# Kernel tuning notes

Hardware: AMD Instinct MI355X
Metric: run time of the kernel (lower is better)

## Reference

```python
import jax, jax.numpy as jnp
import numpy as np

D_MODEL = 768
NUM_HEADS = 6
SPARSITY = 0.1
HEAD_DIM = D_MODEL // NUM_HEADS
SCALE = HEAD_DIM ** -0.5
B, C = 8, 4096


def setup_inputs() -> dict:
    key = jax.random.key(0)
    k1, k2 = jax.random.split(key, 2)
    x = jax.random.normal(k1, (B, C, D_MODEL), dtype=jnp.float32)
    # to_qkv: Linear(d_model, 3*d_model); torch layout W:[out,in], b:[out]
    W = jax.random.normal(k2, (3 * D_MODEL, D_MODEL), dtype=jnp.float32) * (D_MODEL ** -0.5)
    b = jnp.zeros((3 * D_MODEL,), dtype=jnp.float32)
    return {"x": x, "W": W, "b": b}


def reference(x, W, b):
    Bb, Cc, X = x.shape
    H, Dh = NUM_HEADS, HEAD_DIM
    n = Bb * Cc
    qkv = (x.reshape(n, X) @ W.T + b).reshape(n, 3, H, Dh)
    q, k, v = qkv[:, 0], qkv[:, 1], qkv[:, 2]  # each [n, H, Dh]
    # per-token attention across heads: [n, H, H]
    scores = jnp.einsum('nhd,ngd->nhg', q, k) * SCALE
    k_heads = max(1, int(H * SPARSITY))
    topk_scores, topk_idx = jax.lax.top_k(scores, k_heads)  # [n, H, k]
    soft = jax.nn.softmax(topk_scores, axis=-1)
    # sparse_attn @ v == weighted gather of v rows at topk_idx (zeros elsewhere)
    v_g = jnp.take_along_axis(v[:, None, :, :], topk_idx[..., None], axis=2)  # [n, H, k, Dh]
    out = jnp.einsum('nhk,nhkd->nhd', soft, v_g)  # [n, H, Dh]
    # torch: out.transpose(1, 2).reshape(B, C, d_model)  (3D tensor -> swap H and Dh)
    out = jnp.swapaxes(out, 1, 2).reshape(Bb, Cc, X)
    channel_importance = jnp.linalg.norm(out, axis=-1)  # [B, C]
    k_channels = max(1, int(Cc * SPARSITY))
    _, ch_idx = jax.lax.top_k(channel_importance, k_channels)  # [B, k_channels]
    sparse_feat = jnp.take_along_axis(out, ch_idx[:, :, None], axis=1)  # [B, k_channels, d_model]
    return sparse_feat, ch_idx, k_channels
```

## Files before the change

kernel.cpp:

```cpp
#include <hip/hip_runtime.h>
#include <cstdint>
#include <cstddef>

#pragma clang fp contract(off)

#define NROWS 32768
#define NCOLS 2304
#define DMODEL 768
#define QK 1536
#define KCH 409
#define NBATCH 8
#define FEAT_ELEMS ((size_t)NBATCH * KCH * DMODEL)
#define SCALE_F 0.08838834764831845f

#define BM 128
#define BN 128
#define BK 32
#define RS 140

typedef float v4f __attribute__((ext_vector_type(4)));

__device__ __forceinline__ int chunk_off(int c) { return 8 * c + 4 * (c >> 2); }

__global__ __launch_bounds__(256) void gemm_qkv_f32(
    const float* __restrict__ x, const float* __restrict__ W,
    const float* __restrict__ bias, float* __restrict__ qkv)
{
    __shared__ float As[BK * RS];
    __shared__ float Bs[BK * RS];

    const int tid = threadIdx.x;
    const int tx = tid & 15;
    const int ty = tid >> 4;
    const int n0 = blockIdx.x * BN;
    const int m0 = blockIdx.y * BM;

    const int sm = tid >> 3;
    const int t8 = tid & 7;
    const int wsub = sm & 7;
    const int wchk = sm >> 3;

    const float* xa = x + (size_t)(m0 + sm) * DMODEL + t8;
    const float* wb = W + (size_t)(n0 + sm) * DMODEL + t8;

    int co[4];
    #pragma unroll
    for (int i = 0; i < 4; ++i) co[i] = chunk_off(wchk + 4 * i) + wsub;

    float pa[4][4], pb[4][4];
    #pragma unroll
    for (int i = 0; i < 4; ++i)
        #pragma unroll
        for (int j = 0; j < 4; ++j) {
            pa[i][j] = xa[(size_t)(32 * i) * DMODEL + 8 * j];
            pb[i][j] = wb[(size_t)(32 * i) * DMODEL + 8 * j];
        }

    float acc[8][8] = {};

    for (int kt = 0; kt < DMODEL / BK; ++kt) {
        __syncthreads();
        #pragma unroll
        for (int i = 0; i < 4; ++i) {
            #pragma unroll
            for (int j = 0; j < 4; ++j) {
                As[(t8 + 8 * j) * RS + co[i]] = pa[i][j];
                Bs[(t8 + 8 * j) * RS + co[i]] = pb[i][j];
            }
        }
        __syncthreads();

        if (kt + 1 < DMODEL / BK) {
            const int ko = (kt + 1) * BK;
            #pragma unroll
            for (int i = 0; i < 4; ++i)
                #pragma unroll
                for (int j = 0; j < 4; ++j) {
                    pa[i][j] = xa[(size_t)(32 * i) * DMODEL + ko + 8 * j];
                    pb[i][j] = wb[(size_t)(32 * i) * DMODEL + ko + 8 * j];
                }
        }

        const float* Ap = &As[chunk_off(ty)];
        const float* Bp = &Bs[chunk_off(tx)];
        #pragma unroll 8
        for (int k = 0; k < BK; ++k) {
            const v4f a0 = *(const v4f*)(Ap + k * RS);
            const v4f a1 = *(const v4f*)(Ap + k * RS + 4);
            const v4f b0 = *(const v4f*)(Bp + k * RS);
            const v4f b1 = *(const v4f*)(Bp + k * RS + 4);
            const float a[8] = {a0.x, a0.y, a0.z, a0.w, a1.x, a1.y, a1.z, a1.w};
            const float b[8] = {b0.x, b0.y, b0.z, b0.w, b1.x, b1.y, b1.z, b1.w};
            #pragma unroll
            for (int i = 0; i < 8; ++i)
                #pragma unroll
                for (int j = 0; j < 8; ++j)
                    acc[i][j] = fmaf(a[i], b[j], acc[i][j]);
        }
    }

    const int col = n0 + 8 * tx;
    float bcol[8];
    #pragma unroll
    for (int j = 0; j < 8; ++j) bcol[j] = bias[col + j];

    #pragma unroll
    for (int i = 0; i < 8; ++i) {
        const int row = m0 + 8 * ty + i;
        float4 o0, o1;
        o0.x = acc[i][0] + bcol[0];
        o0.y = acc[i][1] + bcol[1];
        o0.z = acc[i][2] + bcol[2];
        o0.w = acc[i][3] + bcol[3];
        o1.x = acc[i][4] + bcol[4];
        o1.y = acc[i][5] + bcol[5];
        o1.z = acc[i][6] + bcol[6];
        o1.w = acc[i][7] + bcol[7];
        *(float4*)(&qkv[(size_t)row * NCOLS + col])     = o0;
        *(float4*)(&qkv[(size_t)row * NCOLS + col + 4]) = o1;
    }
}

__global__ __launch_bounds__(256) void select_and_norm(
    const float* __restrict__ qkv, float* __restrict__ norms,
    uint64_t* __restrict__ gstar)
{
    __shared__ float rowbuf[4][NCOLS];
    __shared__ float sc[4][36];
    __shared__ int   gs_s[4][6];
    __shared__ float sblk[4][8];

    const int tid  = threadIdx.x;
    const int wave = tid >> 6;
    const int lane = tid & 63;
    const int n = blockIdx.x * 4 + wave;

    {
        const float4* src = (const float4*)(qkv + (size_t)n * NCOLS);
        float4* dst = (float4*)(&rowbuf[wave][0]);
        #pragma unroll
        for (int i = 0; i < 9; ++i) dst[lane + 64 * i] = src[lane + 64 * i];
    }
    __syncthreads();

    if (lane < 36) {
        const int h = lane / 6, g = lane % 6;
        const float* qh = &rowbuf[wave][h * 128];
        const float* kh = &rowbuf[wave][768 + g * 128];
        float s = 0.0f;
        for (int d = 0; d < 128; ++d)
            s = s + qh[d] * kh[d];
        sc[wave][lane] = s * SCALE_F;
    }
    __syncthreads();

    if (lane < 6) {
        float best = sc[wave][lane * 6];
        int bg = 0;
        #pragma unroll
        for (int g = 1; g < 6; ++g) {
            const float v = sc[wave][lane * 6 + g];
            if (v > best) { best = v; bg = g; }
        }
        gs_s[wave][lane] = bg;
    }
    __syncthreads();

    if (lane < 8) {
        const float* vr = &rowbuf[wave][QK];
        int gtab[6];
        #pragma unroll
        for (int h = 0; h < 6; ++h) gtab[h] = gs_s[wave][h];

        float r8[8];
        #pragma unroll
        for (int jj = 0; jj < 8; ++jj) {
            const int f = 96 * lane + jj;
            const float v = vr[gtab[f % 6] * 128 + f / 6];
            r8[jj] = v * v;
        }
        for (int i = 8; i < 96; i += 8) {
            #pragma unroll
            for (int jj = 0; jj < 8; ++jj) {
                const int f = 96 * lane + i + jj;
                const float v = vr[gtab[f % 6] * 128 + f / 6];
                r8[jj] = r8[jj] + v * v;
            }
        }
        sblk[wave][lane] = ((r8[0] + r8[1]) + (r8[2] + r8[3]))
                         + ((r8[4] + r8[5]) + (r8[6] + r8[7]));
    }
    __syncthreads();

    if (lane == 0) {
        const float* s = sblk[wave];
        float n2 = ((s[0] + s[1]) + (s[2] + s[3]))
                 + ((s[4] + s[5]) + (s[6] + s[7]));
        norms[n] = sqrtf(n2);
        uint64_t pk = 0;
        #pragma unroll
        for (int h = 0; h < 6; ++h)
            pk |= (uint64_t)gs_s[wave][h] << (8 * h);
        gstar[n] = pk;
    }
}

__global__ __launch_bounds__(256) void topk_channels(
    const float* __restrict__ norms, int* __restrict__ chidx,
    float* __restrict__ out)
{
    __shared__ float vals[4096];
    __shared__ float rv[256];
    __shared__ int   ri[256];
    const int b = blockIdx.x, t = threadIdx.x;

    for (int i = t; i < 4096; i += 256)
        vals[i] = norms[(size_t)b * 4096 + i];
    __syncthreads();

    for (int j = 0; j < KCH; ++j) {
        float best = -1.0f;
        int bi = 0;
        #pragma unroll
        for (int u = 0; u < 16; ++u) {
            const int i = t + 256 * u;
            const float v = vals[i];
            if (v > best) { best = v; bi = i; }
        }
        rv[t] = best; ri[t] = bi;
        __syncthreads();
        for (int s2 = 128; s2 > 0; s2 >>= 1) {
            if (t < s2) {
                const float ov = rv[t + s2]; const int oi = ri[t + s2];
                if (ov > rv[t] || (ov == rv[t] && oi < ri[t])) { rv[t] = ov; ri[t] = oi; }
            }
            __syncthreads();
        }
        if (t == 0) {
            const int w = ri[0];
            chidx[b * KCH + j] = w;
            out[FEAT_ELEMS + (size_t)b * KCH + j] = (float)w;
            vals[w] = -1.0f;
        }
        __syncthreads();
    }
    if (b == 0 && t == 0)
        out[FEAT_ELEMS + (size_t)NBATCH * KCH] = (float)KCH;
}

__global__ __launch_bounds__(256) void gather_sparse(
    const float* __restrict__ qkv, const uint64_t* __restrict__ gstar,
    const int* __restrict__ chidx, float* __restrict__ out)
{
    const int bj = blockIdx.x;
    const int b = bj / KCH;
    const int ch = chidx[bj];
    const int n = b * 4096 + ch;
    const uint64_t pk = gstar[n];
    for (int f = threadIdx.x; f < DMODEL; f += 256) {
        const int h = f % 6;
        const int d = f / 6;
        const int g = (int)((pk >> (8 * h)) & 7u);
        out[(size_t)bj * DMODEL + f] = qkv[(size_t)n * NCOLS + QK + g * 128 + d];
    }
}

extern "C" void kernel_launch(void* const* d_in, const int* in_sizes, int n_in,
                              void* d_out, int out_size, void* d_ws, size_t ws_size,
                              hipStream_t stream)
{
    const float* x    = (const float*)d_in[0];
    const float* W    = (const float*)d_in[1];
    const float* bias = (const float*)d_in[2];
    float* out = (float*)d_out;
    char*  ws  = (char*)d_ws;

    const size_t qkvBytes   = (size_t)NROWS * NCOLS * sizeof(float);
    const size_t normsBytes = (size_t)NROWS * sizeof(float);
    const size_t gstarBytes = (size_t)NROWS * sizeof(uint64_t);
    const size_t chidxBytes = (size_t)NBATCH * KCH * sizeof(int);
    const size_t baseBytes  = qkvBytes + normsBytes + gstarBytes + chidxBytes;
    if (ws_size < baseBytes) return;

    float*    qkv   = (float*)ws;
    float*    norms = (float*)(ws + qkvBytes);
    uint64_t* gstar = (uint64_t*)(ws + qkvBytes + normsBytes);
    int*      chidx = (int*)(ws + qkvBytes + normsBytes + gstarBytes);

    gemm_qkv_f32<<<dim3(NCOLS / BN, NROWS / BM), 256, 0, stream>>>(x, W, bias, qkv);
    select_and_norm<<<NROWS / 4, 256, 0, stream>>>(qkv, norms, gstar);
    topk_channels<<<NBATCH, 256, 0, stream>>>(norms, chidx, out);
    gather_sparse<<<NBATCH * KCH, 256, 0, stream>>>(qkv, gstar, chidx, out);
}
```

Measured before the change: 2.330 ms.

## Use direct global-to-LDS loads with double-buffered shared tiles in QKV GEMM

Replaces the register-staged transposed LDS stores in the fp32 QKV GEMM with global_load_lds DMA of 16-byte chunks into a k-major-by-4 layout. Shared tiles are double-buffered so the next K tile loads while the current one is consumed, leaving one barrier per iteration. The inner loop now reads float4 fragments per 4-k group. It removes VGPR staging and LDS write traffic, at the cost of double the LDS footprint and a changed thread-to-output mapping that must stay consistent with the epilogue.

```diff
diff --git a/kernel.cpp b/kernel.cpp
--- a/kernel.cpp
+++ b/kernel.cpp
@@ -16,87 +16,75 @@
 #define BM 128
 #define BN 128
 #define BK 32
-#define RS 140
 
 typedef float v4f __attribute__((ext_vector_type(4)));
-
-__device__ __forceinline__ int chunk_off(int c) { return 8 * c + 4 * (c >> 2); }
 
 __global__ __launch_bounds__(256) void gemm_qkv_f32(
     const float* __restrict__ x, const float* __restrict__ W,
     const float* __restrict__ bias, float* __restrict__ qkv)
 {
-    __shared__ float As[BK * RS];
-    __shared__ float Bs[BK * RS];
-
-    const int tid = threadIdx.x;
+    __shared__ __align__(16) float As[2][4096];
+    __shared__ __align__(16) float Bs[2][4096];
+
+    const int tid  = threadIdx.x;
+    const int lane = tid & 63;
+    const int wid  = tid >> 6;
     const int tx = tid & 15;
     const int ty = tid >> 4;
     const int n0 = blockIdx.x * BN;
     const int m0 = blockIdx.y * BM;
 
-    const int sm = tid >> 3;
-    const int t8 = tid & 7;
-    const int wsub = sm & 7;
-    const int wchk = sm >> 3;
-
-    const float* xa = x + (size_t)(m0 + sm) * DMODEL + t8;
-    const float* wb = W + (size_t)(n0 + sm) * DMODEL + t8;
-
-    int co[4];
-    #pragma unroll
-    for (int i = 0; i < 4; ++i) co[i] = chunk_off(wchk + 4 * i) + wsub;
-
-    float pa[4][4], pb[4][4];
-    #pragma unroll
-    for (int i = 0; i < 4; ++i)
-        #pragma unroll
-        for (int j = 0; j < 4; ++j) {
-            pa[i][j] = xa[(size_t)(32 * i) * DMODEL + 8 * j];
-            pb[i][j] = wb[(size_t)(32 * i) * DMODEL + 8 * j];
-        }
+    const int rowoff = 8 * (lane & 15) + (lane >> 4);
+    const float* pA0 = x + (size_t)(m0 + rowoff) * DMODEL + 8 * wid;
+    const float* pA1 = x + (size_t)(m0 + rowoff + 4) * DMODEL + 8 * wid;
+    const float* pB0 = W + (size_t)(n0 + rowoff) * DMODEL + 8 * wid;
+    const float* pB1 = W + (size_t)(n0 + rowoff + 4) * DMODEL + 8 * wid;
 
     float acc[8][8] = {};
 
+#define DMA16(gp, lp) \
+    __builtin_amdgcn_global_load_lds( \
+        (const __attribute__((address_space(1))) uint32_t*)(gp), \
+        (__attribute__((address_space(3))) uint32_t*)(lp), 16, 0, 0)
+
+#define STAGE(buf) do { \
+    float* Ab = &As[buf][(2 * wid) * 512]; \
+    float* Bb = &Bs[buf][(2 * wid) * 512]; \
+    DMA16(pA0,     Ab);        DMA16(pA1,     Ab + 256); \
+    DMA16(pA0 + 4, Ab + 512);  DMA16(pA1 + 4, Ab + 768); \
+    DMA16(pB0,     Bb);        DMA16(pB1,     Bb + 256); \
+    DMA16(pB0 + 4, Bb + 512);  DMA16(pB1 + 4, Bb + 768); \
+} while (0)
+
+    STAGE(0);
+    pA0 += BK; pA1 += BK; pB0 += BK; pB1 += BK;
+    __syncthreads();
+
     for (int kt = 0; kt < DMODEL / BK; ++kt) {
+        const int cb = kt & 1;
+        if (kt + 1 < DMODEL / BK) {
+            STAGE(cb ^ 1);
+            pA0 += BK; pA1 += BK; pB0 += BK; pB1 += BK;
+        }
+
+        #pragma unroll
+        for (int g = 0; g < 8; ++g) {
+            const float* Ag = &As[cb][g * 512 + 4 * ty];
+            const float* Bg = &Bs[cb][g * 512 + 4 * tx];
+            v4f a[8], b[8];
+            #pragma unroll
+            for (int i = 0; i < 8; ++i) a[i] = *(const v4f*)(Ag + 64 * i);
+            #pragma unroll
+            for (int j = 0; j < 8; ++j) b[j] = *(const v4f*)(Bg + 64 * j);
+            #pragma unroll
+            for (int kq = 0; kq < 4; ++kq)
+                #pragma unroll
+                for (int i = 0; i < 8; ++i)
+                    #pragma unroll
+                    for (int j = 0; j < 8; ++j)
+                        acc[i][j] = fmaf(a[i][kq], b[j][kq], acc[i][j]);
+        }
         __syncthreads();
-        #pragma unroll
-        for (int i = 0; i < 4; ++i) {
-            #pragma unroll
-            for (int j = 0; j < 4; ++j) {
-                As[(t8 + 8 * j) * RS + co[i]] = pa[i][j];
-                Bs[(t8 + 8 * j) * RS + co[i]] = pb[i][j];
-            }
-        }
-        __syncthreads();
-
-        if (kt + 1 < DMODEL / BK) {
-            const int ko = (kt + 1) * BK;
-            #pragma unroll
-            for (int i = 0; i < 4; ++i)
-                #pragma unroll
-                for (int j = 0; j < 4; ++j) {
-                    pa[i][j] = xa[(size_t)(32 * i) * DMODEL + ko + 8 * j];
-                    pb[i][j] = wb[(size_t)(32 * i) * DMODEL + ko + 8 * j];
-                }
-        }
-
-        const float* Ap = &As[chunk_off(ty)];
-        const float* Bp = &Bs[chunk_off(tx)];
-        #pragma unroll 8
-        for (int k = 0; k < BK; ++k) {
-            const v4f a0 = *(const v4f*)(Ap + k * RS);
-            const v4f a1 = *(const v4f*)(Ap + k * RS + 4);
-            const v4f b0 = *(const v4f*)(Bp + k * RS);
-            const v4f b1 = *(const v4f*)(Bp + k * RS + 4);
-            const float a[8] = {a0.x, a0.y, a0.z, a0.w, a1.x, a1.y, a1.z, a1.w};
-            const float b[8] = {b0.x, b0.y, b0.z, b0.w, b1.x, b1.y, b1.z, b1.w};
-            #pragma unroll
-            for (int i = 0; i < 8; ++i)
-                #pragma unroll
-                for (int j = 0; j < 8; ++j)
-                    acc[i][j] = fmaf(a[i], b[j], acc[i][j]);
-        }
     }
 
     const int col = n0 + 8 * tx;
```

Measured after the change: 2.621 ms. 1.12x slower.
